# Kernel tuning notes

Measured on AMD Instinct MI355X. Metric: run time of the kernel, lower is better.

Reference implementation:

```python
import jax, jax.numpy as jnp
import numpy as np

N_NODES = 50000
NEG_SLOPE = 0.01  # default leaky_relu slope in torch/F.leaky_relu


def sage_gcn_layer(x, src, dst, W, b):
    # DGL SAGEConv with aggregator_type='gcn':
    #   h_neigh[v] = (sum_{(u->v) in E} x[u] + x[v]) / (in_deg(v) + 1)
    #   out = h_neigh @ W + b
    msg = jax.ops.segment_sum(x[src], dst, num_segments=N_NODES)  # [N, d]
    deg = jax.ops.segment_sum(jnp.ones_like(dst, dtype=x.dtype), dst,
                              num_segments=N_NODES)               # [N]
    h = (msg + x) / (deg + 1.0)[:, None]
    return h @ W + b


def setup_inputs() -> dict:
    key = jax.random.key(0)
    ks = jax.random.split(key, 5)
    in_feats, h_feats, num_classes = 128, 128, 32
    n_edges = 800000
    in_feat = jax.random.normal(ks[0], (N_NODES, in_feats), dtype=jnp.float32)
    edges = jax.random.randint(ks[1], (2, n_edges), 0, N_NODES, dtype=jnp.int64)
    W1 = jax.random.normal(ks[2], (in_feats, h_feats), dtype=jnp.float32) / np.sqrt(in_feats)
    b1 = jnp.zeros((h_feats,), dtype=jnp.float32)
    W2 = jax.random.normal(ks[3], (h_feats, num_classes), dtype=jnp.float32) / np.sqrt(h_feats)
    b2 = jnp.zeros((num_classes,), dtype=jnp.float32)
    return {"in_feat": in_feat, "edges": edges, "W1": W1, "b1": b1, "W2": W2, "b2": b2}


def reference(in_feat, edges, W1, b1, W2, b2):
    src, dst = edges[0], edges[1]
    h = sage_gcn_layer(in_feat, src, dst, W1, b1)      # conv1
    h = jnp.where(h >= 0, h, NEG_SLOPE * h)            # leaky_relu
    h = sage_gcn_layer(h, src, dst, W2, b2)            # conv2
    return h
```

## Files before the change

### kernel.cpp

```cpp
#include <hip/hip_runtime.h>

#define N_NODES  50000
#define F_IN     128
#define F_H      128
#define F_OUT    32
#define N_EDGES  800000
#define NEG_SLOPE 0.01f
#define NBUCKET   196
#define EDGE_BLOCKS 784
#define EPB       1024
#define GEMM1_TILES 1563
#define GEMM1_BLOCKS (GEMM1_TILES * 2)

__device__ __forceinline__ float bf2f(unsigned short h) {
    return __uint_as_float(((unsigned)h) << 16);
}
__device__ __forceinline__ unsigned short f2bf(float f) {
    unsigned u = __float_as_uint(f);
    u += 0x7FFF + ((u >> 16) & 1);
    return (unsigned short)(u >> 16);
}

__global__ __launch_bounds__(256) void hist_gemm1_kernel(
    const int* __restrict__ dst, int* __restrict__ counts,
    const float* __restrict__ x, const float* __restrict__ W,
    unsigned short* __restrict__ yb)
{
    __shared__ float Wl[128 * 68];
    __shared__ float Rl[32 * 132];
    int b = blockIdx.x;
    int t = threadIdx.x;

    if (b < EDGE_BLOCKS) {
        int* hist = (int*)Rl;
        for (int i = t; i < NBUCKET; i += 256) hist[i] = 0;
        __syncthreads();
        int base = b * EPB;
        for (int r = 0; r < EPB / 256; ++r) {
            int e = base + r * 256 + t;
            if (e < N_EDGES) atomicAdd(&hist[dst[e] >> 8], 1);
        }
        __syncthreads();
        for (int i = t; i < NBUCKET; i += 256)
            counts[i * EDGE_BLOCKS + b] = hist[i];
        return;
    }

    int g     = b - EDGE_BLOCKS;
    int vb    = (g >> 1) * 32;
    int jbase = (g & 1) * 64;

    for (int i4 = t; i4 < 2048; i4 += 256) {
        int flat = i4 * 4;
        int k  = flat >> 6;
        int jj = flat & 63;
        *(float4*)(Wl + k * 68 + jj) = *(const float4*)(W + k * F_H + jbase + jj);
    }
    for (int i4 = t; i4 < 1024; i4 += 256) {
        int flat = i4 * 4;
        int r = flat >> 7;
        int k = flat & 127;
        int v = vb + r;
        float4 sv = (v < N_NODES) ? *(const float4*)(x + (size_t)v * F_IN + k)
                                  : make_float4(0.f, 0.f, 0.f, 0.f);
        *(float4*)(Rl + r * 132 + k) = sv;
    }
    __syncthreads();

    int j0 = (t & 15) * 4;
    int r0 = (t >> 4) * 2;
    float acc[2][4] = {{0.f,0.f,0.f,0.f},{0.f,0.f,0.f,0.f}};
    for (int k = 0; k < 128; ++k) {
        float4 w = *(const float4*)(Wl + k * 68 + j0);
        float s0 = Rl[(r0    ) * 132 + k];
        float s1 = Rl[(r0 + 1) * 132 + k];
        acc[0][0] += s0 * w.x; acc[0][1] += s0 * w.y;
        acc[0][2] += s0 * w.z; acc[0][3] += s0 * w.w;
        acc[1][0] += s1 * w.x; acc[1][1] += s1 * w.y;
        acc[1][2] += s1 * w.z; acc[1][3] += s1 * w.w;
    }
    for (int i = 0; i < 2; ++i) {
        int v = vb + r0 + i;
        if (v >= N_NODES) continue;
        ushort4 o;
        o.x = f2bf(acc[i][0]); o.y = f2bf(acc[i][1]);
        o.z = f2bf(acc[i][2]); o.w = f2bf(acc[i][3]);
        *(ushort4*)(yb + (size_t)v * F_H + jbase + j0) = o;
    }
}


__global__ __launch_bounds__(256) void scan_cols_kernel(
    int* __restrict__ counts, int* __restrict__ bucket_total)
{
    __shared__ int c[256];
    int t = threadIdx.x;
    int carry = 0;
    for (int ch = 0; ch < (EDGE_BLOCKS + 255) / 256; ++ch) {
        int ci = ch * 256 + t;
        int cv = (ci < EDGE_BLOCKS) ? counts[blockIdx.x * EDGE_BLOCKS + ci] : 0;
        c[t] = cv;
        __syncthreads();
        for (int off = 1; off < 256; off <<= 1) {
            int a = c[t];
            int add = (t >= off) ? c[t - off] : 0;
            __syncthreads();
            c[t] = a + add;
            __syncthreads();
        }
        if (ci < EDGE_BLOCKS)
            counts[blockIdx.x * EDGE_BLOCKS + ci] = carry + c[t] - cv;
        carry += c[255];
        __syncthreads();
    }
    if (t == 0) bucket_total[blockIdx.x] = carry;
}

__global__ __launch_bounds__(256) void bucket_base_kernel(
    const int* __restrict__ bucket_total, int* __restrict__ bucket_base)
{
    __shared__ int s[256];
    int t = threadIdx.x;
    int v = (t < NBUCKET) ? bucket_total[t] : 0;
    s[t] = v;
    __syncthreads();
    for (int off = 1; off < 256; off <<= 1) {
        int a = s[t];
        int add = (t >= off) ? s[t - off] : 0;
        __syncthreads();
        s[t] = a + add;
        __syncthreads();
    }
    if (t < NBUCKET) bucket_base[t] = s[t] - v;
    if (t == 0) bucket_base[NBUCKET] = s[NBUCKET - 1];
}

__global__ __launch_bounds__(256) void bin_kernel(
    const int* __restrict__ src, const int* __restrict__ dst,
    const int* __restrict__ rel, const int* __restrict__ bucket_base,
    unsigned int* __restrict__ bins)
{
    __shared__ int pos[NBUCKET];
    int blk = blockIdx.x;
    int t = threadIdx.x;
    for (int i = t; i < NBUCKET; i += 256)
        pos[i] = bucket_base[i] + rel[i * EDGE_BLOCKS + blk];
    __syncthreads();
    int base = blk * EPB;
    for (int r = 0; r < EPB / 256; ++r) {
        int e = base + r * 256 + t;
        if (e < N_EDGES) {
            int d = dst[e];
            int sy = src[e];
            int p = atomicAdd(&pos[d >> 8], 1);
            bins[p] = ((unsigned)d << 16) | (unsigned)sy;
        }
    }
}

__global__ __launch_bounds__(256) void bucket_sort_kernel(
    const unsigned int* __restrict__ bins, const int* __restrict__ bucket_base,
    int* __restrict__ row_ptr, int* __restrict__ csr)
{
    __shared__ int cnt[256];
    __shared__ int cur[256];
    int b = blockIdx.x;
    int t = threadIdx.x;
    int nlo = b * 256;
    int beg = bucket_base[b];
    int end = bucket_base[b + 1];
    cnt[t] = 0;
    __syncthreads();
    for (int i = beg + t; i < end; i += 256)
        atomicAdd(&cnt[(bins[i] >> 16) & 255], 1);
    __syncthreads();
    int v = cnt[t];
    cur[t] = v;
    __syncthreads();
    for (int off = 1; off < 256; off <<= 1) {
        int a = cur[t];
        int add = (t >= off) ? cur[t - off] : 0;
        __syncthreads();
        cur[t] = a + add;
        __syncthreads();
    }
    int start = beg + cur[t] - v;
    int node = nlo + t;
    if (node < N_NODES) row_ptr[node] = start;
    cur[t] = start;
    if (b == 0 && t == 0) row_ptr[N_NODES] = N_EDGES;
    __syncthreads();
    for (int i = beg + t; i < end; i += 256) {
        unsigned w = bins[i];
        int dl = (w >> 16) & 255;
        int p = atomicAdd(&cur[dl], 1);
        csr[p] = (int)(w & 0xFFFFu);
    }
}


__global__ __launch_bounds__(256) void aggregate128_kernel(
    const unsigned short* __restrict__ yb, const int* __restrict__ row_ptr,
    const int* __restrict__ csr, const float* __restrict__ b1,
    unsigned short* __restrict__ h1b)
{
    int gw = (blockIdx.x * 256 + threadIdx.x) >> 5;
    int l4 = (threadIdx.x & 31) * 4;
    if (gw >= N_NODES) return;
    int beg = row_ptr[gw];
    int end = row_ptr[gw + 1];
    ushort4 us = *(const ushort4*)(yb + (size_t)gw * 128 + l4);
    float ax = bf2f(us.x), ay = bf2f(us.y), az = bf2f(us.z), aw = bf2f(us.w);
    float bx = 0.f, by = 0.f, bz = 0.f, bw = 0.f;
    int p = beg;
    for (; p + 3 < end; p += 4) {
        int s0 = csr[p], s1 = csr[p + 1], s2 = csr[p + 2], s3 = csr[p + 3];
        ushort4 u0 = *(const ushort4*)(yb + (size_t)s0 * 128 + l4);
        ushort4 u1 = *(const ushort4*)(yb + (size_t)s1 * 128 + l4);
        ushort4 u2 = *(const ushort4*)(yb + (size_t)s2 * 128 + l4);
        ushort4 u3 = *(const ushort4*)(yb + (size_t)s3 * 128 + l4);
        ax += bf2f(u0.x) + bf2f(u2.x); ay += bf2f(u0.y) + bf2f(u2.y);
        az += bf2f(u0.z) + bf2f(u2.z); aw += bf2f(u0.w) + bf2f(u2.w);
        bx += bf2f(u1.x) + bf2f(u3.x); by += bf2f(u1.y) + bf2f(u3.y);
        bz += bf2f(u1.z) + bf2f(u3.z); bw += bf2f(u1.w) + bf2f(u3.w);
    }
    for (; p < end; ++p) {
        int s0 = csr[p];
        ushort4 u0 = *(const ushort4*)(yb + (size_t)s0 * 128 + l4);
        ax += bf2f(u0.x); ay += bf2f(u0.y); az += bf2f(u0.z); aw += bf2f(u0.w);
    }
    float rec = 1.0f / (float)(end - beg + 1);
    float4 bb = *(const float4*)(b1 + l4);
    float vx = (ax + bx) * rec + bb.x;
    float vy = (ay + by) * rec + bb.y;
    float vz = (az + bz) * rec + bb.z;
    float vw = (aw + bw) * rec + bb.w;
    vx = (vx >= 0.f) ? vx : NEG_SLOPE * vx;
    vy = (vy >= 0.f) ? vy : NEG_SLOPE * vy;
    vz = (vz >= 0.f) ? vz : NEG_SLOPE * vz;
    vw = (vw >= 0.f) ? vw : NEG_SLOPE * vw;
    ushort4 o;
    o.x = f2bf(vx); o.y = f2bf(vy); o.z = f2bf(vz); o.w = f2bf(vw);
    *(ushort4*)(h1b + (size_t)gw * 128 + l4) = o;
}

__global__ __launch_bounds__(256) void aggregate32_kernel(
    const unsigned short* __restrict__ zb, const int* __restrict__ row_ptr,
    const int* __restrict__ csr, const float* __restrict__ b2,
    float* __restrict__ out)
{
    int g  = (blockIdx.x * 256 + threadIdx.x) >> 3;
    int l4 = (threadIdx.x & 7) * 4;
    if (g >= N_NODES) return;
    int beg = row_ptr[g];
    int end = row_ptr[g + 1];
    ushort4 us = *(const ushort4*)(zb + (size_t)g * 32 + l4);
    float ax = bf2f(us.x), ay = bf2f(us.y), az = bf2f(us.z), aw = bf2f(us.w);
    float bx = 0.f, by = 0.f, bz = 0.f, bw = 0.f;
    int p = beg;
    for (; p + 3 < end; p += 4) {
        int s0 = csr[p], s1 = csr[p + 1], s2 = csr[p + 2], s3 = csr[p + 3];
        ushort4 u0 = *(const ushort4*)(zb + (size_t)s0 * 32 + l4);
        ushort4 u1 = *(const ushort4*)(zb + (size_t)s1 * 32 + l4);
        ushort4 u2 = *(const ushort4*)(zb + (size_t)s2 * 32 + l4);
        ushort4 u3 = *(const ushort4*)(zb + (size_t)s3 * 32 + l4);
        ax += bf2f(u0.x) + bf2f(u2.x); ay += bf2f(u0.y) + bf2f(u2.y);
        az += bf2f(u0.z) + bf2f(u2.z); aw += bf2f(u0.w) + bf2f(u2.w);
        bx += bf2f(u1.x) + bf2f(u3.x); by += bf2f(u1.y) + bf2f(u3.y);
        bz += bf2f(u1.z) + bf2f(u3.z); bw += bf2f(u1.w) + bf2f(u3.w);
    }
    for (; p < end; ++p) {
        int s0 = csr[p];
        ushort4 u0 = *(const ushort4*)(zb + (size_t)s0 * 32 + l4);
        ax += bf2f(u0.x); ay += bf2f(u0.y); az += bf2f(u0.z); aw += bf2f(u0.w);
    }
    float rec = 1.0f / (float)(end - beg + 1);
    float4 bb = *(const float4*)(b2 + l4);
    float4 o;
    o.x = (ax + bx) * rec + bb.x;
    o.y = (ay + by) * rec + bb.y;
    o.z = (az + bz) * rec + bb.z;
    o.w = (aw + bw) * rec + bb.w;
    *(float4*)(out + (size_t)g * 32 + l4) = o;
}

__global__ __launch_bounds__(256) void gemm2z_kernel(
    const unsigned short* __restrict__ h1b, const float* __restrict__ W,
    unsigned short* __restrict__ zb)
{
    __shared__ float Wl[128 * 36];
    __shared__ float Rl[64 * 132];
    int t  = threadIdx.x;
    int vb = blockIdx.x * 64;

    for (int i4 = t; i4 < 1024; i4 += 256) {
        int flat = i4 * 4;
        int k  = flat >> 5;
        int jj = flat & 31;
        *(float4*)(Wl + k * 36 + jj) = *(const float4*)(W + k * F_OUT + jj);
    }
    for (int i8 = t; i8 < 1024; i8 += 256) {
        int r = i8 >> 4;
        int k = (i8 & 15) * 8;
        int v = vb + r;
        float f[8];
        if (v < N_NODES) {
            uint4 u = *(const uint4*)(h1b + (size_t)v * F_H + k);
            f[0] = __uint_as_float(u.x << 16);
            f[1] = __uint_as_float(u.x & 0xFFFF0000u);
            f[2] = __uint_as_float(u.y << 16);
            f[3] = __uint_as_float(u.y & 0xFFFF0000u);
            f[4] = __uint_as_float(u.z << 16);
            f[5] = __uint_as_float(u.z & 0xFFFF0000u);
            f[6] = __uint_as_float(u.w << 16);
            f[7] = __uint_as_float(u.w & 0xFFFF0000u);
        } else {
            for (int q = 0; q < 8; ++q) f[q] = 0.f;
        }
        for (int q = 0; q < 8; ++q) Rl[r * 132 + k + q] = f[q];
    }
    __syncthreads();

    int j0 = (t & 7) * 4;
    int r0 = (t >> 3) * 2;
    float acc[2][4] = {{0.f,0.f,0.f,0.f},{0.f,0.f,0.f,0.f}};
    for (int k = 0; k < 128; ++k) {
        float4 w = *(const float4*)(Wl + k * 36 + j0);
        float s0 = Rl[(r0    ) * 132 + k];
        float s1 = Rl[(r0 + 1) * 132 + k];
        acc[0][0] += s0 * w.x; acc[0][1] += s0 * w.y;
        acc[0][2] += s0 * w.z; acc[0][3] += s0 * w.w;
        acc[1][0] += s1 * w.x; acc[1][1] += s1 * w.y;
        acc[1][2] += s1 * w.z; acc[1][3] += s1 * w.w;
    }
    for (int i = 0; i < 2; ++i) {
        int v = vb + r0 + i;
        if (v >= N_NODES) continue;
        ushort4 o;
        o.x = f2bf(acc[i][0]); o.y = f2bf(acc[i][1]);
        o.z = f2bf(acc[i][2]); o.w = f2bf(acc[i][3]);
        *(ushort4*)(zb + (size_t)v * F_OUT + j0) = o;
    }
}

__global__ __launch_bounds__(256) void scatter_kernel(
    const float* __restrict__ x, const int* __restrict__ src,
    const int* __restrict__ dst, float* __restrict__ msg,
    float* __restrict__ deg, int nE)
{
    int tid  = blockIdx.x * 256 + threadIdx.x;
    int e    = tid >> 5;
    int lane = tid & 31;
    if (e >= nE) return;
    int s = src[e];
    int d = dst[e];
    if (deg != nullptr && lane == 0) atomicAdd(&deg[d], 1.0f);
    float4 v = *(const float4*)(x + (size_t)s * F_IN + lane * 4);
    float* mp = msg + (size_t)d * F_IN + lane * 4;
    atomicAdd(mp + 0, v.x);
    atomicAdd(mp + 1, v.y);
    atomicAdd(mp + 2, v.z);
    atomicAdd(mp + 3, v.w);
}

__global__ __launch_bounds__(256) void normalize_kernel(
    const float* __restrict__ self, const float* __restrict__ deg,
    float* __restrict__ msg)
{
    int idx = blockIdx.x * 256 + threadIdx.x;
    int v = idx >> 5;
    int c = (idx & 31) * 4;
    if (v >= N_NODES) return;
    float rec = 1.0f / (deg[v] + 1.0f);
    float4 m = *(const float4*)(msg  + (size_t)v * 128 + c);
    float4 s = *(const float4*)(self + (size_t)v * 128 + c);
    m.x = (m.x + s.x) * rec;
    m.y = (m.y + s.y) * rec;
    m.z = (m.z + s.z) * rec;
    m.w = (m.w + s.w) * rec;
    *(float4*)(msg + (size_t)v * 128 + c) = m;
}

__global__ __launch_bounds__(256) void gemm1_kernel(
    const float* __restrict__ msg, const float* __restrict__ W,
    const float* __restrict__ b, float* __restrict__ h)
{
    __shared__ float Wl[128 * 68];
    __shared__ float Rl[32 * 132];
    int t     = threadIdx.x;
    int vb    = blockIdx.x * 32;
    int jbase = blockIdx.y * 64;
    for (int i4 = t; i4 < 2048; i4 += 256) {
        int flat = i4 * 4;
        int k  = flat >> 6;
        int jj = flat & 63;
        *(float4*)(Wl + k * 68 + jj) = *(const float4*)(W + k * F_H + jbase + jj);
    }
    for (int i4 = t; i4 < 1024; i4 += 256) {
        int flat = i4 * 4;
        int r = flat >> 7;
        int k = flat & 127;
        int v = vb + r;
        float4 sv = (v < N_NODES) ? *(const float4*)(msg + (size_t)v * F_IN + k)
                                  : make_float4(0.f, 0.f, 0.f, 0.f);
        *(float4*)(Rl + r * 132 + k) = sv;
    }
    __syncthreads();
    int j0 = (t & 15) * 4;
    int r0 = (t >> 4) * 2;
    float acc[2][4] = {{0.f,0.f,0.f,0.f},{0.f,0.f,0.f,0.f}};
    for (int k = 0; k < 128; ++k) {
        float4 w = *(const float4*)(Wl + k * 68 + j0);
        float s0 = Rl[(r0    ) * 132 + k];
        float s1 = Rl[(r0 + 1) * 132 + k];
        acc[0][0] += s0 * w.x; acc[0][1] += s0 * w.y;
        acc[0][2] += s0 * w.z; acc[0][3] += s0 * w.w;
        acc[1][0] += s1 * w.x; acc[1][1] += s1 * w.y;
        acc[1][2] += s1 * w.z; acc[1][3] += s1 * w.w;
    }
    for (int i = 0; i < 2; ++i) {
        int v = vb + r0 + i;
        if (v >= N_NODES) continue;
        float4 o;
        o.x = acc[i][0] + b[jbase + j0 + 0];
        o.y = acc[i][1] + b[jbase + j0 + 1];
        o.z = acc[i][2] + b[jbase + j0 + 2];
        o.w = acc[i][3] + b[jbase + j0 + 3];
        o.x = (o.x >= 0.f) ? o.x : NEG_SLOPE * o.x;
        o.y = (o.y >= 0.f) ? o.y : NEG_SLOPE * o.y;
        o.z = (o.z >= 0.f) ? o.z : NEG_SLOPE * o.z;
        o.w = (o.w >= 0.f) ? o.w : NEG_SLOPE * o.w;
        *(float4*)(h + (size_t)v * F_H + jbase + j0) = o;
    }
}

__global__ __launch_bounds__(256) void gemm2_kernel(
    const float* __restrict__ msg, const float* __restrict__ W,
    const float* __restrict__ b, float* __restrict__ out)
{
    __shared__ float Wl[128 * 36];
    __shared__ float Rl[64 * 132];
    int t  = threadIdx.x;
    int vb = blockIdx.x * 64;
    for (int i4 = t; i4 < 1024; i4 += 256) {
        int flat = i4 * 4;
        int k  = flat >> 5;
        int jj = flat & 31;
        *(float4*)(Wl + k * 36 + jj) = *(const float4*)(W + k * F_OUT + jj);
    }
    for (int i4 = t; i4 < 2048; i4 += 256) {
        int flat = i4 * 4;
        int r = flat >> 7;
        int k = flat & 127;
        int v = vb + r;
        float4 sv = (v < N_NODES) ? *(const float4*)(msg + (size_t)v * F_H + k)
                                  : make_float4(0.f, 0.f, 0.f, 0.f);
        *(float4*)(Rl + r * 132 + k) = sv;
    }
    __syncthreads();
    int j0 = (t & 7) * 4;
    int r0 = (t >> 3) * 2;
    float acc[2][4] = {{0.f,0.f,0.f,0.f},{0.f,0.f,0.f,0.f}};
    for (int k = 0; k < 128; ++k) {
        float4 w = *(const float4*)(Wl + k * 36 + j0);
        float s0 = Rl[(r0    ) * 132 + k];
        float s1 = Rl[(r0 + 1) * 132 + k];
        acc[0][0] += s0 * w.x; acc[0][1] += s0 * w.y;
        acc[0][2] += s0 * w.z; acc[0][3] += s0 * w.w;
        acc[1][0] += s1 * w.x; acc[1][1] += s1 * w.y;
        acc[1][2] += s1 * w.z; acc[1][3] += s1 * w.w;
    }
    for (int i = 0; i < 2; ++i) {
        int v = vb + r0 + i;
        if (v >= N_NODES) continue;
        float4 o;
        o.x = acc[i][0] + b[j0 + 0];
        o.y = acc[i][1] + b[j0 + 1];
        o.z = acc[i][2] + b[j0 + 2];
        o.w = acc[i][3] + b[j0 + 3];
        *(float4*)(out + (size_t)v * F_OUT + j0) = o;
    }
}

extern "C" void kernel_launch(void* const* d_in, const int* in_sizes, int n_in,
                              void* d_out, int out_size, void* d_ws, size_t ws_size,
                              hipStream_t stream)
{
    const float* x     = (const float*)d_in[0];
    const int*   edges = (const int*)d_in[1];
    const float* W1    = (const float*)d_in[2];
    const float* b1    = (const float*)d_in[3];
    const float* W2    = (const float*)d_in[4];
    const float* b2    = (const float*)d_in[5];
    float* out = (float*)d_out;

    const int* src = edges;
    const int* dst = edges + N_EDGES;

    const size_t INT_WORDS = 256ull + 256ull + 50432ull + 800000ull
                           + 153664ull + 800000ull;
    const size_t FAST_BYTES = INT_WORDS * 4
                            + (6400000ull + 6400000ull + 1600000ull) * 2;

    if (ws_size >= FAST_BYTES) {
        int*   bucket_total = (int*)d_ws;
        int*   bucket_base  = bucket_total + 256;
        int*   row_ptr      = bucket_base + 256;
        int*   csr          = row_ptr + 50432;
        int*   counts       = csr + 800000;
        unsigned int* bins  = (unsigned int*)(counts + 153664);
        unsigned short* yb  = (unsigned short*)(bins + 800000);
        unsigned short* h1b = yb + 6400000;
        unsigned short* zb  = h1b + 6400000;

        hist_gemm1_kernel<<<EDGE_BLOCKS + GEMM1_BLOCKS, 256, 0, stream>>>(
            dst, counts, x, W1, yb);
        scan_cols_kernel<<<NBUCKET, 256, 0, stream>>>(counts, bucket_total);
        bucket_base_kernel<<<1, 256, 0, stream>>>(bucket_total, bucket_base);
        bin_kernel<<<EDGE_BLOCKS, 256, 0, stream>>>(src, dst, counts,
                                                    bucket_base, bins);
        bucket_sort_kernel<<<NBUCKET, 256, 0, stream>>>(bins, bucket_base,
                                                        row_ptr, csr);
        int ab1 = (N_NODES * 32 + 255) / 256;
        aggregate128_kernel<<<ab1, 256, 0, stream>>>(yb, row_ptr, csr, b1, h1b);
        gemm2z_kernel<<<(N_NODES + 63) / 64, 256, 0, stream>>>(h1b, W2, zb);
        int ab2 = (N_NODES * 8 + 255) / 256;
        aggregate32_kernel<<<ab2, 256, 0, stream>>>(zb, row_ptr, csr, b2, out);
    } else {
        float* deg = (float*)d_ws;
        float* msg = deg + 50176;
        float* h1  = msg + (size_t)N_NODES * F_H;

        hipMemsetAsync(d_ws, 0, (50176 + (size_t)N_NODES * F_H) * sizeof(float), stream);
        int sb = (N_EDGES * 32 + 255) / 256;
        int nb = (N_NODES * 32 + 255) / 256;

        scatter_kernel<<<sb, 256, 0, stream>>>(x, src, dst, msg, deg, N_EDGES);
        normalize_kernel<<<nb, 256, 0, stream>>>(x, deg, msg);
        gemm1_kernel<<<dim3((N_NODES + 31) / 32, 2), 256, 0, stream>>>(msg, W1, b1, h1);

        hipMemsetAsync(msg, 0, (size_t)N_NODES * F_H * sizeof(float), stream);
        scatter_kernel<<<sb, 256, 0, stream>>>(h1, src, dst, msg, nullptr, N_EDGES);
        normalize_kernel<<<nb, 256, 0, stream>>>(h1, deg, msg);
        gemm2_kernel<<<(N_NODES + 63) / 64, 256, 0, stream>>>(msg, W2, b2, out);
    }
}
```

Measured before the change: 194.5 us.

## Use bf16 MFMA for both dense GEMMs with pre-converted weights

Replaces the scalar FP32 shared-memory GEMMs in the fused hist/gemm1 kernel and in gemm2z with bf16 MFMA 16x16x32 instructions. A small prep kernel converts W1 and W2 to bf16 in the workspace first. Each wave loads its B fragments straight from global memory into registers, and the GEMM1 block now covers 64 rows by all 128 columns. This cuts FP32 FMA compute cost but adds an extra launch, and it rounds x and the weights to bf16, which costs accuracy. Output stores are now scalar 16-bit writes.

```diff
diff --git a/kernel.cpp b/kernel.cpp
--- a/kernel.cpp
+++ b/kernel.cpp
@@ -9,8 +9,11 @@
 #define NBUCKET   196
 #define EDGE_BLOCKS 784
 #define EPB       1024
-#define GEMM1_TILES 1563
-#define GEMM1_BLOCKS (GEMM1_TILES * 2)
+#define GEMM1_BLOCKS 782
+#define GEMM2_BLOCKS 391
+
+typedef short bf16x8 __attribute__((ext_vector_type(8)));
+typedef float f32x4  __attribute__((ext_vector_type(4)));
 
 __device__ __forceinline__ float bf2f(unsigned short h) {
     return __uint_as_float(((unsigned)h) << 16);
@@ -21,18 +24,38 @@
     return (unsigned short)(u >> 16);
 }
 
+__global__ __launch_bounds__(256) void prep_kernel(
+    const float* __restrict__ W1, const float* __restrict__ W2,
+    unsigned short* __restrict__ W1b, unsigned short* __restrict__ W2b)
+{
+    int idx = (blockIdx.x * 256 + threadIdx.x) * 4;
+    if (idx < 16384) {
+        float4 v = *(const float4*)(W1 + idx);
+        ushort4 o;
+        o.x = f2bf(v.x); o.y = f2bf(v.y); o.z = f2bf(v.z); o.w = f2bf(v.w);
+        *(ushort4*)(W1b + idx) = o;
+    } else {
+        int j = idx - 16384;
+        if (j < 4096) {
+            float4 v = *(const float4*)(W2 + j);
+            ushort4 o;
+            o.x = f2bf(v.x); o.y = f2bf(v.y); o.z = f2bf(v.z); o.w = f2bf(v.w);
+            *(ushort4*)(W2b + j) = o;
+        }
+    }
+}
+
 __global__ __launch_bounds__(256) void hist_gemm1_kernel(
     const int* __restrict__ dst, int* __restrict__ counts,
-    const float* __restrict__ x, const float* __restrict__ W,
+    const float* __restrict__ x, const unsigned short* __restrict__ W1b,
     unsigned short* __restrict__ yb)
 {
-    __shared__ float Wl[128 * 68];
-    __shared__ float Rl[32 * 132];
+    __shared__ alignas(16) unsigned short Xl[64 * 136];
     int b = blockIdx.x;
     int t = threadIdx.x;
 
     if (b < EDGE_BLOCKS) {
-        int* hist = (int*)Rl;
+        int* hist = (int*)Xl;
         for (int i = t; i < NBUCKET; i += 256) hist[i] = 0;
         __syncthreads();
         int base = b * EPB;
@@ -46,49 +69,63 @@
         return;
     }
 
-    int g     = b - EDGE_BLOCKS;
-    int vb    = (g >> 1) * 32;
-    int jbase = (g & 1) * 64;
+    int g  = b - EDGE_BLOCKS;
+    int vb = g * 64;
 
     for (int i4 = t; i4 < 2048; i4 += 256) {
-        int flat = i4 * 4;
-        int k  = flat >> 6;
-        int jj = flat & 63;
-        *(float4*)(Wl + k * 68 + jj) = *(const float4*)(W + k * F_H + jbase + jj);
-    }
-    for (int i4 = t; i4 < 1024; i4 += 256) {
         int flat = i4 * 4;
         int r = flat >> 7;
         int k = flat & 127;
         int v = vb + r;
-        float4 sv = (v < N_NODES) ? *(const float4*)(x + (size_t)v * F_IN + k)
+        float4 xv = (v < N_NODES) ? *(const float4*)(x + (size_t)v * 128 + k)
                                   : make_float4(0.f, 0.f, 0.f, 0.f);
-        *(float4*)(Rl + r * 132 + k) = sv;
-    }
-    __syncthreads();
-
-    int j0 = (t & 15) * 4;
-    int r0 = (t >> 4) * 2;
-    float acc[2][4] = {{0.f,0.f,0.f,0.f},{0.f,0.f,0.f,0.f}};
-    for (int k = 0; k < 128; ++k) {
-        float4 w = *(const float4*)(Wl + k * 68 + j0);
-        float s0 = Rl[(r0    ) * 132 + k];
-        float s1 = Rl[(r0 + 1) * 132 + k];
-        acc[0][0] += s0 * w.x; acc[0][1] += s0 * w.y;
-        acc[0][2] += s0 * w.z; acc[0][3] += s0 * w.w;
-        acc[1][0] += s1 * w.x; acc[1][1] += s1 * w.y;
-        acc[1][2] += s1 * w.z; acc[1][3] += s1 * w.w;
-    }
-    for (int i = 0; i < 2; ++i) {
-        int v = vb + r0 + i;
-        if (v >= N_NODES) continue;
         ushort4 o;
-        o.x = f2bf(acc[i][0]); o.y = f2bf(acc[i][1]);
-        o.z = f2bf(acc[i][2]); o.w = f2bf(acc[i][3]);
-        *(ushort4*)(yb + (size_t)v * F_H + jbase + j0) = o;
-    }
-}
-
+        o.x = f2bf(xv.x); o.y = f2bf(xv.y); o.z = f2bf(xv.z); o.w = f2bf(xv.w);
+        *(ushort4*)(Xl + r * 136 + k) = o;
+    }
+
+    int wv   = t >> 6;
+    int lane = t & 63;
+    int quad = lane >> 4;
+    int lc   = lane & 15;
+    int c0   = wv * 32;
+
+    bf16x8 bfr[2][4];
+    for (int ct = 0; ct < 2; ++ct)
+        for (int ks = 0; ks < 4; ++ks) {
+            bf16x8 tmp;
+            #pragma unroll
+            for (int j = 0; j < 8; ++j)
+                tmp[j] = (short)W1b[(ks * 32 + quad * 8 + j) * 128 + c0 + ct * 16 + lc];
+            bfr[ct][ks] = tmp;
+        }
+
+    __syncthreads();
+
+    f32x4 acc[4][2];
+    for (int rt = 0; rt < 4; ++rt)
+        for (int ct = 0; ct < 2; ++ct)
+            acc[rt][ct] = (f32x4){0.f, 0.f, 0.f, 0.f};
+
+    for (int rt = 0; rt < 4; ++rt) {
+        int row = rt * 16 + lc;
+        #pragma unroll
+        for (int ks = 0; ks < 4; ++ks) {
+            bf16x8 af = *(const bf16x8*)(Xl + row * 136 + ks * 32 + quad * 8);
+            acc[rt][0] = __builtin_amdgcn_mfma_f32_16x16x32_bf16(af, bfr[0][ks], acc[rt][0], 0, 0, 0);
+            acc[rt][1] = __builtin_amdgcn_mfma_f32_16x16x32_bf16(af, bfr[1][ks], acc[rt][1], 0, 0, 0);
+        }
+    }
+
+    for (int rt = 0; rt < 4; ++rt)
+        for (int ct = 0; ct < 2; ++ct)
+            #pragma unroll
+            for (int r = 0; r < 4; ++r) {
+                int grow = vb + rt * 16 + quad * 4 + r;
+                if (grow < N_NODES)
+                    yb[(size_t)grow * 128 + c0 + ct * 16 + lc] = f2bf(acc[rt][ct][r]);
+            }
+}
 
 __global__ __launch_bounds__(256) void scan_cols_kernel(
     int* __restrict__ counts, int* __restrict__ bucket_total)
@@ -197,7 +234,6 @@
         csr[p] = (int)(w & 0xFFFFu);
     }
 }
-
 
 __global__ __launch_bounds__(256) void aggregate128_kernel(
     const unsigned short* __restrict__ yb, const int* __restrict__ row_ptr,
@@ -285,62 +321,50 @@
 }
 
 __global__ __launch_bounds__(256) void gemm2z_kernel(
-    const unsigned short* __restrict__ h1b, const float* __restrict__ W,
-    unsigned short* __restrict__ zb)
-{
-    __shared__ float Wl[128 * 36];
-    __shared__ float Rl[64 * 132];
-    int t  = threadIdx.x;
-    int vb = blockIdx.x * 64;
-
-    for (int i4 = t; i4 < 1024; i4 += 256) {
-        int flat = i4 * 4;
-        int k  = flat >> 5;
-        int jj = flat & 31;
-        *(float4*)(Wl + k * 36 + jj) = *(const float4*)(W + k * F_OUT + jj);
-    }
-    for (int i8 = t; i8 < 1024; i8 += 256) {
-        int r = i8 >> 4;
-        int k = (i8 & 15) * 8;
-        int v = vb + r;
-        float f[8];
-        if (v < N_NODES) {
-            uint4 u = *(const uint4*)(h1b + (size_t)v * F_H + k);
-            f[0] = __uint_as_float(u.x << 16);
-            f[1] = __uint_as_float(u.x & 0xFFFF0000u);
-            f[2] = __uint_as_float(u.y << 16);
-            f[3] = __uint_as_float(u.y & 0xFFFF0000u);
-            f[4] = __uint_as_float(u.z << 16);
-            f[5] = __uint_as_float(u.z & 0xFFFF0000u);
-            f[6] = __uint_as_float(u.w << 16);
-            f[7] = __uint_as_float(u.w & 0xFFFF0000u);
-        } else {
-            for (int q = 0; q < 8; ++q) f[q] = 0.f;
-        }
-        for (int q = 0; q < 8; ++q) Rl[r * 132 + k + q] = f[q];
-    }
-    __syncthreads();
-
-    int j0 = (t & 7) * 4;
-    int r0 = (t >> 3) * 2;
-    float acc[2][4] = {{0.f,0.f,0.f,0.f},{0.f,0.f,0.f,0.f}};
-    for (int k = 0; k < 128; ++k) {
-        float4 w = *(const float4*)(Wl + k * 36 + j0);
-        float s0 = Rl[(r0    ) * 132 + k];
-        float s1 = Rl[(r0 + 1) * 132 + k];
-        acc[0][0] += s0 * w.x; acc[0][1] += s0 * w.y;
-        acc[0][2] += s0 * w.z; acc[0][3] += s0 * w.w;
-        acc[1][0] += s1 * w.x; acc[1][1] += s1 * w.y;
-        acc[1][2] += s1 * w.z; acc[1][3] += s1 * w.w;
-    }
-    for (int i = 0; i < 2; ++i) {
-        int v = vb + r0 + i;
-        if (v >= N_NODES) continue;
-        ushort4 o;
-        o.x = f2bf(acc[i][0]); o.y = f2bf(acc[i][1]);
-        o.z = f2bf(acc[i][2]); o.w = f2bf(acc[i][3]);
-        *(ushort4*)(zb + (size_t)v * F_OUT + j0) = o;
-    }
+    const unsigned short* __restrict__ h1b,
+    const unsigned short* __restrict__ W2b, unsigned short* __restrict__ zb)
+{
+    int t    = threadIdx.x;
+    int wv   = t >> 6;
+    int lane = t & 63;
+    int quad = lane >> 4;
+    int lc   = lane & 15;
+
+    bf16x8 bfr[2][4];
+    for (int ct = 0; ct < 2; ++ct)
+        for (int ks = 0; ks < 4; ++ks) {
+            bf16x8 tmp;
+            #pragma unroll
+            for (int j = 0; j < 8; ++j)
+                tmp[j] = (short)W2b[(ks * 32 + quad * 8 + j) * 32 + ct * 16 + lc];
+            bfr[ct][ks] = tmp;
+        }
+
+    f32x4 acc[2][2];
+    for (int rt = 0; rt < 2; ++rt)
+        for (int ct = 0; ct < 2; ++ct)
+            acc[rt][ct] = (f32x4){0.f, 0.f, 0.f, 0.f};
+
+    int vb = blockIdx.x * 128 + wv * 32;
+    for (int rt = 0; rt < 2; ++rt) {
+        int row = vb + rt * 16 + lc;
+        int vrow = (row < N_NODES) ? row : 0;
+        #pragma unroll
+        for (int ks = 0; ks < 4; ++ks) {
+            bf16x8 af = *(const bf16x8*)(h1b + (size_t)vrow * 128 + ks * 32 + quad * 8);
+            acc[rt][0] = __builtin_amdgcn_mfma_f32_16x16x32_bf16(af, bfr[0][ks], acc[rt][0], 0, 0, 0);
+            acc[rt][1] = __builtin_amdgcn_mfma_f32_16x16x32_bf16(af, bfr[1][ks], acc[rt][1], 0, 0, 0);
+        }
+    }
+
+    for (int rt = 0; rt < 2; ++rt)
+        for (int ct = 0; ct < 2; ++ct)
+            #pragma unroll
+            for (int r = 0; r < 4; ++r) {
+                int grow = vb + rt * 16 + quad * 4 + r;
+                if (grow < N_NODES)
+                    zb[(size_t)grow * 32 + ct * 16 + lc] = f2bf(acc[rt][ct][r]);
+            }
 }
 
 __global__ __launch_bounds__(256) void scatter_kernel(
@@ -499,8 +523,8 @@
 
     const size_t INT_WORDS = 256ull + 256ull + 50432ull + 800000ull
                            + 153664ull + 800000ull;
-    const size_t FAST_BYTES = INT_WORDS * 4
-                            + (6400000ull + 6400000ull + 1600000ull) * 2;
+    const size_t SHORTS = 6400000ull + 6400000ull + 1600000ull + 16384ull + 4096ull;
+    const size_t FAST_BYTES = INT_WORDS * 4 + SHORTS * 2;
 
     if (ws_size >= FAST_BYTES) {
         int*   bucket_total = (int*)d_ws;
@@ -512,9 +536,12 @@
         unsigned short* yb  = (unsigned short*)(bins + 800000);
         unsigned short* h1b = yb + 6400000;
         unsigned short* zb  = h1b + 6400000;
-
+        unsigned short* W1b = zb + 1600000;
+        unsigned short* W2b = W1b + 16384;
+
+        prep_kernel<<<20, 256, 0, stream>>>(W1, W2, W1b, W2b);
         hist_gemm1_kernel<<<EDGE_BLOCKS + GEMM1_BLOCKS, 256, 0, stream>>>(
-            dst, counts, x, W1, yb);
+            dst, counts, x, W1b, yb);
         scan_cols_kernel<<<NBUCKET, 256, 0, stream>>>(counts, bucket_total);
         bucket_base_kernel<<<1, 256, 0, stream>>>(bucket_total, bucket_base);
         bin_kernel<<<EDGE_BLOCKS, 256, 0, stream>>>(src, dst, counts,
@@ -523,7 +550,7 @@
                                                         row_ptr, csr);
         int ab1 = (N_NODES * 32 + 255) / 256;
         aggregate128_kernel<<<ab1, 256, 0, stream>>>(yb, row_ptr, csr, b1, h1b);
-        gemm2z_kernel<<<(N_NODES + 63) / 64, 256, 0, stream>>>(h1b, W2, zb);
+        gemm2z_kernel<<<GEMM2_BLOCKS, 256, 0, stream>>>(h1b, W2b, zb);
         int ab2 = (N_NODES * 8 + 255) / 256;
         aggregate32_kernel<<<ab2, 256, 0, stream>>>(zb, row_ptr, csr, b2, out);
     } else {
```

Result: faster. 168.9 us (-13.2%).
